# Kernel optimization log

Hardware: AMD Instinct MI355X
Metric: run time of the kernel (lower is better)

The kernel has to match this reference:

```python
import jax, jax.numpy as jnp
import numpy as np

B, H, W, C = 2, 64, 64, 256
NH, K = 8, 7  # num_heads, neighborhood kernel size


def setup_inputs() -> dict:
    key = jax.random.key(0)
    ks = jax.random.split(key, 8)
    xav = lambda k, shape: jax.random.normal(k, shape, jnp.float32) * np.sqrt(2.0 / (shape[0] + shape[1])).astype(np.float32)
    return {
        "x": jax.random.normal(ks[0], (B, H, W, C), jnp.float32),
        "norm1_g": jnp.ones((C,), jnp.float32),
        "norm1_b": jnp.zeros((C,), jnp.float32),
        "qkv_w": xav(ks[1], (3 * C, C)),
        "qkv_b": jnp.zeros((3 * C,), jnp.float32),
        "rpb": jax.random.normal(ks[2], (NH, 2 * K - 1, 2 * K - 1), jnp.float32) * 0.02,
        "proj_w": xav(ks[3], (C, C)),
        "proj_b": jnp.zeros((C,), jnp.float32),
        "norm2_g": jnp.ones((C,), jnp.float32),
        "norm2_b": jnp.zeros((C,), jnp.float32),
        "fc1_w": xav(ks[4], (4 * C, C)),
        "fc1_b": jnp.zeros((4 * C,), jnp.float32),
        "fc2_w": xav(ks[5], (C, 4 * C)),
        "fc2_b": jnp.zeros((C,), jnp.float32),
    }


def _layernorm(x, g, b, eps=1e-5):
    m = x.mean(-1, keepdims=True)
    v = jnp.mean((x - m) ** 2, axis=-1, keepdims=True)
    return (x - m) * jax.lax.rsqrt(v + eps) * g + b


def _nat2d(x, qkv_w, qkv_b, rpb, proj_w, proj_b):
    """Neighborhood attention 2D (NATTEN semantics: edge-clamped k x k windows,
    relative positional bias indexed by key_pos - query_pos + k - 1)."""
    b, h, w, c = x.shape
    nh = rpb.shape[0]
    k = (rpb.shape[1] + 1) // 2
    dh = c // nh
    qkv = (x @ qkv_w.T + qkv_b).reshape(b, h, w, 3, nh, dh)
    q = qkv[..., 0, :, :] * (dh ** -0.5)  # [b,h,w,nh,dh]
    kk = qkv[..., 1, :, :]
    vv = qkv[..., 2, :, :]
    # edge-clamped window starts per query row/col
    starts_h = jnp.clip(jnp.arange(h) - k // 2, 0, h - k)
    starts_w = jnp.clip(jnp.arange(w) - k // 2, 0, w - k)
    idx_h = starts_h[:, None] + jnp.arange(k)  # [h,k] key row indices
    idx_w = starts_w[:, None] + jnp.arange(k)  # [w,k] key col indices
    # gather neighborhoods -> [b,h,w,k,k,nh,dh]
    knb = kk[:, idx_h][:, :, :, idx_w].transpose(0, 1, 3, 2, 4, 5, 6)
    vnb = vv[:, idx_h][:, :, :, idx_w].transpose(0, 1, 3, 2, 4, 5, 6)
    attn = jnp.einsum('bijhd,bijklhd->bijhkl', q, knb)  # [b,h,w,nh,k,k]
    # relative positional bias: index = key - query + (k-1) in [0, 2k-2]
    rb_h = idx_h - jnp.arange(h)[:, None] + (k - 1)  # [h,k]
    rb_w = idx_w - jnp.arange(w)[:, None] + (k - 1)  # [w,k]
    bias = rpb[:, rb_h][:, :, :, rb_w]  # [nh,h,k,w,k]
    bias = bias.transpose(1, 3, 0, 2, 4)  # [h,w,nh,k,k]
    attn = jax.nn.softmax((attn + bias).reshape(b, h, w, nh, k * k), axis=-1)
    out = jnp.einsum('bijhn,bijnhd->bijhd', attn, vnb.reshape(b, h, w, k * k, nh, dh))
    return out.reshape(b, h, w, c) @ proj_w.T + proj_b


def reference(x, norm1_g, norm1_b, qkv_w, qkv_b, rpb, proj_w, proj_b,
              norm2_g, norm2_b, fc1_w, fc1_b, fc2_w, fc2_b):
    # norm -> neighborhood attention -> residual
    x = x + _nat2d(_layernorm(x, norm1_g, norm1_b), qkv_w, qkv_b, rpb, proj_w, proj_b)
    # norm -> MLP (gelu) -> residual
    hdn = _layernorm(x, norm2_g, norm2_b)
    hdn = jax.nn.gelu(hdn @ fc1_w.T + fc1_b, approximate=False)
    return x + (hdn @ fc2_w.T + fc2_b)
```

## Files before the change

### kernel.cpp

```cpp
#include <hip/hip_runtime.h>

typedef __attribute__((ext_vector_type(8))) short bf16x8;
typedef __attribute__((ext_vector_type(4))) float f32x4;
typedef unsigned short u16;

__device__ __forceinline__ float bf2f(u16 u) {
    return __builtin_bit_cast(float, ((unsigned int)u) << 16);
}
__device__ __forceinline__ u16 f2bf(float f) {
    unsigned int x = __builtin_bit_cast(unsigned int, f);
    x += 0x7FFFu + ((x >> 16) & 1u);
    return (u16)(x >> 16);
}

typedef const __attribute__((address_space(1))) void* gas_t;
typedef __attribute__((address_space(3))) void* las_t;
__device__ __forceinline__ void load_lds16(const u16* g, u16* l) {
    __builtin_amdgcn_global_load_lds((gas_t)g, (las_t)l, 16, 0, 0);
}

__global__ __launch_bounds__(256) void prep_kernel(
    const float* __restrict__ s0, const float* __restrict__ s1,
    const float* __restrict__ s2, const float* __restrict__ s3,
    u16* __restrict__ dst,
    const float* __restrict__ x, const float* __restrict__ g,
    const float* __restrict__ b, u16* __restrict__ y)
{
    if (blockIdx.x < 768) {
        const int i4 = (blockIdx.x * 256 + threadIdx.x) * 4;
        const float* src;
        int off;
        if      (i4 < 196608) { src = s0; off = i4; }
        else if (i4 < 262144) { src = s1; off = i4 - 196608; }
        else if (i4 < 524288) { src = s2; off = i4 - 262144; }
        else                  { src = s3; off = i4 - 524288; }
        float4 v = *(const float4*)(src + off);
        ushort4 o;
        o.x = f2bf(v.x); o.y = f2bf(v.y); o.z = f2bf(v.z); o.w = f2bf(v.w);
        *(ushort4*)(dst + i4) = o;
        return;
    }
    const int tok  = (blockIdx.x - 768) * 4 + (threadIdx.x >> 6);
    const int lane = threadIdx.x & 63;
    float4 v = *(const float4*)(x + (size_t)tok * 256 + lane * 4);
    float s  = v.x + v.y + v.z + v.w;
    float sq = v.x*v.x + v.y*v.y + v.z*v.z + v.w*v.w;
    #pragma unroll
    for (int off = 32; off; off >>= 1) {
        s  += __shfl_xor(s, off);
        sq += __shfl_xor(sq, off);
    }
    float mean = s * (1.0f / 256.0f);
    float var  = sq * (1.0f / 256.0f) - mean * mean;
    float rs   = rsqrtf(var + 1e-5f);
    float4 gv = *(const float4*)(g + lane * 4);
    float4 bv = *(const float4*)(b + lane * 4);
    ushort4 o;
    o.x = f2bf((v.x - mean) * rs * gv.x + bv.x);
    o.y = f2bf((v.y - mean) * rs * gv.y + bv.y);
    o.z = f2bf((v.z - mean) * rs * gv.z + bv.z);
    o.w = f2bf((v.w - mean) * rs * gv.w + bv.w);
    *(ushort4*)(y + (size_t)tok * 256 + lane * 4) = o;
}

template<int BM, int BN, int N, int K, int EPI>
__global__ __launch_bounds__(256) void gemm(
    const u16* __restrict__ A, const u16* __restrict__ W,
    const float* __restrict__ bias, const float* __restrict__ res,
    void* __restrict__ outv,
    const float* __restrict__ g2, const float* __restrict__ b2,
    u16* __restrict__ out2)
{
    constexpr int WMT = BM / 32;
    constexpr int WNT = BN / 32;
    constexpr int AR  = BM / 32;
    constexpr int BR  = BN / 32;

    __shared__ u16 As[BM * 64];
    __shared__ u16 Bs[BN * 64];
    __shared__ float red[2][2][16][2];
    const int tid  = threadIdx.x;
    const int lane = tid & 63;
    const int wave = tid >> 6;
    const int m0   = blockIdx.x * BM;
    const int n0   = blockIdx.y * BN;
    const int wm0  = (wave >> 1) * (BM / 2);
    const int wn0  = (wave & 1) * (BN / 2);

    f32x4 acc[WMT][WNT];
    #pragma unroll
    for (int mt = 0; mt < WMT; ++mt)
        #pragma unroll
        for (int nt = 0; nt < WNT; ++nt)
            acc[mt][nt] = (f32x4){0.f, 0.f, 0.f, 0.f};

    int soffA[AR];
    #pragma unroll
    for (int r = 0; r < AR; ++r) {
        const int s   = r * 256 + tid;
        const int row = s >> 3;
        const int c   = (s & 7) ^ (row & 7);
        soffA[r] = row * K + c * 8;
    }
    int soffB[BR];
    #pragma unroll
    for (int r = 0; r < BR; ++r) {
        const int s   = r * 256 + tid;
        const int row = s >> 3;
        const int c   = (s & 7) ^ (row & 7);
        soffB[r] = row * K + c * 8;
    }
    const int fr = lane & 15;
    const int fc = lane >> 4;

    for (int k0 = 0; k0 < K; k0 += 64) {
        __syncthreads();
        #pragma unroll
        for (int r = 0; r < AR; ++r)
            load_lds16(A + (size_t)m0 * K + k0 + soffA[r], As + (r * 256 + tid) * 8);
        #pragma unroll
        for (int r = 0; r < BR; ++r)
            load_lds16(W + (size_t)n0 * K + k0 + soffB[r], Bs + (r * 256 + tid) * 8);
        __syncthreads();
        #pragma unroll
        for (int ks = 0; ks < 2; ++ks) {
            bf16x8 af[WMT], bw[WNT];
            #pragma unroll
            for (int mt = 0; mt < WMT; ++mt) {
                const int rr   = wm0 + mt * 16 + fr;
                const int phys = (ks * 4 + fc) ^ (rr & 7);
                af[mt] = *(const bf16x8*)(As + rr * 64 + phys * 8);
            }
            #pragma unroll
            for (int nt = 0; nt < WNT; ++nt) {
                const int rr   = wn0 + nt * 16 + fr;
                const int phys = (ks * 4 + fc) ^ (rr & 7);
                bw[nt] = *(const bf16x8*)(Bs + rr * 64 + phys * 8);
            }
            #pragma unroll
            for (int mt = 0; mt < WMT; ++mt)
                #pragma unroll
                for (int nt = 0; nt < WNT; ++nt)
                    acc[mt][nt] = __builtin_amdgcn_mfma_f32_16x16x32_bf16(af[mt], bw[nt], acc[mt][nt], 0, 0, 0);
        }
    }

    const int col = lane & 15;
    const int rb  = (lane >> 4) * 4;

    if (EPI == 4) {
        float vv[WNT][4];
        float s[4]  = {0.f, 0.f, 0.f, 0.f};
        float sq[4] = {0.f, 0.f, 0.f, 0.f};
        #pragma unroll
        for (int nt = 0; nt < WNT; ++nt) {
            const int n  = n0 + wn0 + nt * 16 + col;
            const float bv = bias[n];
            #pragma unroll
            for (int r = 0; r < 4; ++r) {
                const int m = m0 + wm0 + rb + r;
                float v = acc[0][nt][r] + bv + res[(size_t)m * N + n];
                ((float*)outv)[(size_t)m * N + n] = v;
                vv[nt][r] = v;
                s[r]  += v;
                sq[r] += v * v;
            }
        }
        #pragma unroll
        for (int off = 1; off < 16; off <<= 1) {
            #pragma unroll
            for (int r = 0; r < 4; ++r) {
                s[r]  += __shfl_xor(s[r], off);
                sq[r] += __shfl_xor(sq[r], off);
            }
        }
        if ((lane & 15) == 0) {
            #pragma unroll
            for (int r = 0; r < 4; ++r) {
                red[wave >> 1][wave & 1][rb + r][0] = s[r];
                red[wave >> 1][wave & 1][rb + r][1] = sq[r];
            }
        }
        __syncthreads();
        float mean[4], rs[4];
        #pragma unroll
        for (int r = 0; r < 4; ++r) {
            float ts  = red[wave >> 1][0][rb + r][0] + red[wave >> 1][1][rb + r][0];
            float tsq = red[wave >> 1][0][rb + r][1] + red[wave >> 1][1][rb + r][1];
            mean[r] = ts * (1.0f / 256.0f);
            float var = tsq * (1.0f / 256.0f) - mean[r] * mean[r];
            rs[r] = rsqrtf(var + 1e-5f);
        }
        #pragma unroll
        for (int nt = 0; nt < WNT; ++nt) {
            const int n  = n0 + wn0 + nt * 16 + col;
            const float gv = g2[n];
            const float bv2 = b2[n];
            #pragma unroll
            for (int r = 0; r < 4; ++r) {
                const int m = m0 + wm0 + rb + r;
                out2[(size_t)m * 256 + n] = f2bf((vv[nt][r] - mean[r]) * rs[r] * gv + bv2);
            }
        }
        return;
    }

    #pragma unroll
    for (int nt = 0; nt < WNT; ++nt) {
        const int n  = n0 + wn0 + nt * 16 + col;
        const float bv = bias[n];
        #pragma unroll
        for (int mt = 0; mt < WMT; ++mt) {
            #pragma unroll
            for (int r = 0; r < 4; ++r) {
                const int m = m0 + wm0 + mt * 16 + rb + r;
                float v = acc[mt][nt][r] + bv;
                if (EPI == 1) {
                    if (n < 256) v *= 0.1767766952966369f;
                    ((u16*)outv)[(size_t)m * N + n] = f2bf(v);
                }
                if (EPI == 2) {
                    v += res[(size_t)m * N + n];
                    ((float*)outv)[(size_t)m * N + n] = v;
                }
                if (EPI == 3) {
                    v = 0.5f * v * (1.0f + erff(v * 0.7071067811865475f));
                    ((u16*)outv)[(size_t)m * N + n] = f2bf(v);
                }
            }
        }
    }
}

__global__ __launch_bounds__(256, 2) void attn_tile_kernel(
    const u16* __restrict__ qkv, const float* __restrict__ rpb,
    u16* __restrict__ out)
{
    __shared__ u16   kv[100 * 64];
    __shared__ u16   qs[16 * 32];
    __shared__ float probs[16 * 66];

    const int tid  = threadIdx.x;
    const int bb   = blockIdx.x >> 8;
    const int rem  = blockIdx.x & 255;
    const int ti0  = (rem >> 4) << 2;
    const int tj0  = (rem & 15) << 2;
    const int oh   = min(max(ti0 - 3, 0), 54);
    const int ow   = min(max(tj0 - 3, 0), 54);
    const int tokbase = bb * 4096;

    int off_kv[4];
    #pragma unroll
    for (int r = 0; r < 4; ++r) {
        const int s  = r * 256 + tid;
        const int t  = s >> 3;
        const int cs = s & 7;
        const int c  = cs ^ (t & 7);
        const int tr = t / 10, tc = t - tr * 10;
        const int tokg = tokbase + (oh + tr) * 64 + (ow + tc);
        off_kv[r] = tokg * 768 + 256 + ((c & 4) << 6) + (c & 3) * 8;
    }
    const int tq   = tid >> 2;
    const int qoff = (tokbase + (ti0 + (tq >> 2)) * 64 + (tj0 + (tq & 3))) * 768
                   + (tid & 3) * 8;

    const int token = tid >> 4;
    const int part  = tid & 15;
    const int li = token >> 2, lj = token & 3;
    const int i  = ti0 + li,   j  = tj0 + lj;
    const int sh = min(max(i - 3, 0), 57);
    const int sw = min(max(j - 3, 0), 57);
    const int rowbase  = (sh - oh) * 10 + (sw - ow);
    const int rb_const = (sh - i + 6) * 13 + (sw - j + 6);
    const size_t outbase = (size_t)(tokbase + i * 64 + j) * 256 + part * 2;

    for (int h = 0; h < 8; ++h) {
        __syncthreads();
        const int hoff = h * 32;
        #pragma unroll
        for (int r = 0; r < 3; ++r)
            load_lds16(qkv + off_kv[r] + hoff, kv + (r * 256 + tid) * 8);
        if (tid < 32)
            load_lds16(qkv + off_kv[3] + hoff, kv + (768 + tid) * 8);
        if (tid < 64)
            load_lds16(qkv + qoff + hoff, qs + tid * 8);
        __syncthreads();

        float qv[32];
        #pragma unroll
        for (int c = 0; c < 4; ++c) {
            bf16x8 v = *(const bf16x8*)(qs + token * 32 + c * 8);
            #pragma unroll
            for (int e = 0; e < 8; ++e) qv[c * 8 + e] = bf2f((u16)v[e]);
        }

        float sc[4];
        #pragma unroll
        for (int sidx = 0; sidx < 4; ++sidx) {
            const int n = part + sidx * 16;
            if (n < 49) {
                const int kh = n / 7, kw = n - (n / 7) * 7;
                const int hidx = rowbase + kh * 10 + kw;
                float acc = rpb[h * 169 + rb_const + kh * 13 + kw];
                #pragma unroll
                for (int c = 0; c < 4; ++c) {
                    const int slot = (hidx << 3) + (c ^ (hidx & 7));
                    bf16x8 kk = *(const bf16x8*)(kv + slot * 8);
                    #pragma unroll
                    for (int e = 0; e < 8; ++e)
                        acc += qv[c * 8 + e] * bf2f((u16)kk[e]);
                }
                sc[sidx] = acc;
            } else {
                sc[sidx] = -1e30f;
            }
        }
        float mx = fmaxf(fmaxf(sc[0], sc[1]), fmaxf(sc[2], sc[3]));
        #pragma unroll
        for (int off = 1; off < 16; off <<= 1) mx = fmaxf(mx, __shfl_xor(mx, off));
        float ex[4], ssum = 0.f;
        #pragma unroll
        for (int sidx = 0; sidx < 4; ++sidx) {
            ex[sidx] = __expf(sc[sidx] - mx);
            ssum += ex[sidx];
        }
        #pragma unroll
        for (int off = 1; off < 16; off <<= 1) ssum += __shfl_xor(ssum, off);
        const float inv = 1.0f / ssum;
        #pragma unroll
        for (int sidx = 0; sidx < 4; ++sidx)
            probs[token * 66 + part + sidx * 16] = ex[sidx] * inv;
        __syncthreads();

        float o0 = 0.f, o1 = 0.f;
        const int vchunk = 4 + (part >> 2);
        const int vsub   = (part & 3) * 2;
        #pragma unroll
        for (int kh = 0; kh < 7; ++kh) {
            #pragma unroll
            for (int kw = 0; kw < 7; ++kw) {
                const int n    = kh * 7 + kw;
                const int hidx = rowbase + kh * 10 + kw;
                const float p  = probs[token * 66 + n];
                const int slot = (hidx << 3) + (vchunk ^ (hidx & 7));
                const unsigned int vv = *(const unsigned int*)(kv + slot * 8 + vsub);
                o0 += p * bf2f((u16)(vv & 0xffffu));
                o1 += p * bf2f((u16)(vv >> 16));
            }
        }
        ushort2 ov;
        ov.x = f2bf(o0); ov.y = f2bf(o1);
        *(ushort2*)(out + outbase + hoff) = ov;
    }
}

extern "C" void kernel_launch(void* const* d_in, const int* in_sizes, int n_in,
                              void* d_out, int out_size, void* d_ws, size_t ws_size,
                              hipStream_t stream)
{
    const float* x      = (const float*)d_in[0];
    const float* n1g    = (const float*)d_in[1];
    const float* n1b    = (const float*)d_in[2];
    const float* qkv_w  = (const float*)d_in[3];
    const float* qkv_b  = (const float*)d_in[4];
    const float* rpb    = (const float*)d_in[5];
    const float* proj_w = (const float*)d_in[6];
    const float* proj_b = (const float*)d_in[7];
    const float* n2g    = (const float*)d_in[8];
    const float* n2b    = (const float*)d_in[9];
    const float* fc1_w  = (const float*)d_in[10];
    const float* fc1_b  = (const float*)d_in[11];
    const float* fc2_w  = (const float*)d_in[12];
    const float* fc2_b  = (const float*)d_in[13];
    float* out = (float*)d_out;

    char* wsb = (char*)d_ws;
    u16*   wbf   = (u16*)wsb;
    u16*   qkvW  = wbf;
    u16*   projW = wbf + 196608;
    u16*   fc1W  = wbf + 262144;
    u16*   fc2W  = wbf + 524288;
    u16*   ln1   = (u16*)(wsb + 1572864);
    u16*   attn  = ln1;
    u16*   qkvB  = (u16*)(wsb + 5767168);
    u16*   ln2   = qkvB;
    u16*   hbuf  = (u16*)(wsb + 9961472);
    float* x1    = (float*)(wsb + 26738688);

    dim3 blk(256);
    prep_kernel<<<2816, blk, 0, stream>>>(qkv_w, proj_w, fc1_w, fc2_w, wbf,
                                          x, n1g, n1b, ln1);
    gemm<64, 64, 768, 256, 1><<<dim3(128, 12), blk, 0, stream>>>(ln1, qkvW, qkv_b, nullptr, qkvB, nullptr, nullptr, nullptr);
    attn_tile_kernel<<<512, blk, 0, stream>>>(qkvB, rpb, attn);
    gemm<32, 256, 256, 256, 4><<<dim3(256, 1), blk, 0, stream>>>(attn, projW, proj_b, x, x1, n2g, n2b, ln2);
    gemm<64, 64, 1024, 256, 3><<<dim3(128, 16), blk, 0, stream>>>(ln2, fc1W, fc1_b, nullptr, hbuf, nullptr, nullptr, nullptr);
    gemm<64, 64, 256, 1024, 2><<<dim3(128, 4), blk, 0, stream>>>(hbuf, fc2W, fc2_b, x1, out, nullptr, nullptr, nullptr);
}
```

Before: 160.1 us.

## Fuse output projection, residual and LayerNorm2 into the attention tile kernel

The attention kernel now keeps its 16-token by 256-channel output in shared memory, using a swizzled layout. It then runs the proj GEMM with MFMA directly from there, reading the proj weights straight from global memory, and applies the bias, residual and LayerNorm2 epilogue before writing x1 and ln2. This removes one kernel launch and the global write and reread of the attention output. In exchange, only 512 blocks each redo a 16x256x256 GEMM with uncached global weight loads, and ln2 moves to a separate workspace region because qkvB can no longer be overwritten.

After: 159.9 us. No clear change (-0.1%).

```diff
diff --git a/kernel.cpp b/kernel.cpp
--- a/kernel.cpp
+++ b/kernel.cpp
@@ -67,9 +67,7 @@
 __global__ __launch_bounds__(256) void gemm(
     const u16* __restrict__ A, const u16* __restrict__ W,
     const float* __restrict__ bias, const float* __restrict__ res,
-    void* __restrict__ outv,
-    const float* __restrict__ g2, const float* __restrict__ b2,
-    u16* __restrict__ out2)
+    void* __restrict__ outv)
 {
     constexpr int WMT = BM / 32;
     constexpr int WNT = BN / 32;
@@ -78,7 +76,6 @@
 
     __shared__ u16 As[BM * 64];
     __shared__ u16 Bs[BN * 64];
-    __shared__ float red[2][2][16][2];
     const int tid  = threadIdx.x;
     const int lane = tid & 63;
     const int wave = tid >> 6;
@@ -147,64 +144,6 @@
 
     const int col = lane & 15;
     const int rb  = (lane >> 4) * 4;
-
-    if (EPI == 4) {
-        float vv[WNT][4];
-        float s[4]  = {0.f, 0.f, 0.f, 0.f};
-        float sq[4] = {0.f, 0.f, 0.f, 0.f};
-        #pragma unroll
-        for (int nt = 0; nt < WNT; ++nt) {
-            const int n  = n0 + wn0 + nt * 16 + col;
-            const float bv = bias[n];
-            #pragma unroll
-            for (int r = 0; r < 4; ++r) {
-                const int m = m0 + wm0 + rb + r;
-                float v = acc[0][nt][r] + bv + res[(size_t)m * N + n];
-                ((float*)outv)[(size_t)m * N + n] = v;
-                vv[nt][r] = v;
-                s[r]  += v;
-                sq[r] += v * v;
-            }
-        }
-        #pragma unroll
-        for (int off = 1; off < 16; off <<= 1) {
-            #pragma unroll
-            for (int r = 0; r < 4; ++r) {
-                s[r]  += __shfl_xor(s[r], off);
-                sq[r] += __shfl_xor(sq[r], off);
-            }
-        }
-        if ((lane & 15) == 0) {
-            #pragma unroll
-            for (int r = 0; r < 4; ++r) {
-                red[wave >> 1][wave & 1][rb + r][0] = s[r];
-                red[wave >> 1][wave & 1][rb + r][1] = sq[r];
-            }
-        }
-        __syncthreads();
-        float mean[4], rs[4];
-        #pragma unroll
-        for (int r = 0; r < 4; ++r) {
-            float ts  = red[wave >> 1][0][rb + r][0] + red[wave >> 1][1][rb + r][0];
-            float tsq = red[wave >> 1][0][rb + r][1] + red[wave >> 1][1][rb + r][1];
-            mean[r] = ts * (1.0f / 256.0f);
-            float var = tsq * (1.0f / 256.0f) - mean[r] * mean[r];
-            rs[r] = rsqrtf(var + 1e-5f);
-        }
-        #pragma unroll
-        for (int nt = 0; nt < WNT; ++nt) {
-            const int n  = n0 + wn0 + nt * 16 + col;
-            const float gv = g2[n];
-            const float bv2 = b2[n];
-            #pragma unroll
-            for (int r = 0; r < 4; ++r) {
-                const int m = m0 + wm0 + rb + r;
-                out2[(size_t)m * 256 + n] = f2bf((vv[nt][r] - mean[r]) * rs[r] * gv + bv2);
-            }
-        }
-        return;
-    }
-
     #pragma unroll
     for (int nt = 0; nt < WNT; ++nt) {
         const int n  = n0 + wn0 + nt * 16 + col;
@@ -232,13 +171,18 @@
     }
 }
 
-__global__ __launch_bounds__(256, 2) void attn_tile_kernel(
+__global__ __launch_bounds__(256, 2) void attn_proj_kernel(
     const u16* __restrict__ qkv, const float* __restrict__ rpb,
-    u16* __restrict__ out)
+    const u16* __restrict__ projW, const float* __restrict__ proj_b,
+    const float* __restrict__ xres, const float* __restrict__ g2,
+    const float* __restrict__ b2, float* __restrict__ x1,
+    u16* __restrict__ ln2)
 {
     __shared__ u16   kv[100 * 64];
     __shared__ u16   qs[16 * 32];
     __shared__ float probs[16 * 66];
+    __shared__ u16   ao[16 * 256];
+    __shared__ float red[4][16][2];
 
     const int tid  = threadIdx.x;
     const int bb   = blockIdx.x >> 8;
@@ -272,7 +216,6 @@
     const int sw = min(max(j - 3, 0), 57);
     const int rowbase  = (sh - oh) * 10 + (sw - ow);
     const int rb_const = (sh - i + 6) * 13 + (sw - j + 6);
-    const size_t outbase = (size_t)(tokbase + i * 64 + j) * 256 + part * 2;
 
     for (int h = 0; h < 8; ++h) {
         __syncthreads();
@@ -350,7 +293,88 @@
         }
         ushort2 ov;
         ov.x = f2bf(o0); ov.y = f2bf(o1);
-        *(ushort2*)(out + outbase + hoff) = ov;
+        const int cch = h * 4 + (part >> 2);
+        const int pch = cch ^ (token & 7);
+        *(ushort2*)(ao + token * 256 + pch * 8 + (part & 3) * 2) = ov;
+    }
+    __syncthreads();
+
+    const int lane = tid & 63;
+    const int wave = tid >> 6;
+    const int fr   = lane & 15;
+    const int fc   = lane >> 4;
+    const int n0w  = wave * 64;
+    f32x4 pacc[4];
+    #pragma unroll
+    for (int nt = 0; nt < 4; ++nt) pacc[nt] = (f32x4){0.f, 0.f, 0.f, 0.f};
+    #pragma unroll
+    for (int ks = 0; ks < 8; ++ks) {
+        const int physA = (ks * 4 + fc) ^ (fr & 7);
+        bf16x8 af = *(const bf16x8*)(ao + fr * 256 + physA * 8);
+        #pragma unroll
+        for (int nt = 0; nt < 4; ++nt) {
+            const int n = n0w + nt * 16 + fr;
+            bf16x8 bw = *(const bf16x8*)(projW + (size_t)n * 256 + ks * 32 + fc * 8);
+            pacc[nt] = __builtin_amdgcn_mfma_f32_16x16x32_bf16(af, bw, pacc[nt], 0, 0, 0);
+        }
+    }
+
+    const int col = lane & 15;
+    const int rb  = (lane >> 4) * 4;
+    float vv[4][4];
+    float s[4]  = {0.f, 0.f, 0.f, 0.f};
+    float sq[4] = {0.f, 0.f, 0.f, 0.f};
+    #pragma unroll
+    for (int nt = 0; nt < 4; ++nt) {
+        const int n = n0w + nt * 16 + col;
+        const float bv = proj_b[n];
+        #pragma unroll
+        for (int r = 0; r < 4; ++r) {
+            const int t = rb + r;
+            const size_t gi = (size_t)(tokbase + (ti0 + (t >> 2)) * 64 + (tj0 + (t & 3))) * 256 + n;
+            float v = pacc[nt][r] + bv + xres[gi];
+            x1[gi] = v;
+            vv[nt][r] = v;
+            s[r]  += v;
+            sq[r] += v * v;
+        }
+    }
+    #pragma unroll
+    for (int off = 1; off < 16; off <<= 1) {
+        #pragma unroll
+        for (int r = 0; r < 4; ++r) {
+            s[r]  += __shfl_xor(s[r], off);
+            sq[r] += __shfl_xor(sq[r], off);
+        }
+    }
+    if (col == 0) {
+        #pragma unroll
+        for (int r = 0; r < 4; ++r) {
+            red[wave][rb + r][0] = s[r];
+            red[wave][rb + r][1] = sq[r];
+        }
+    }
+    __syncthreads();
+    float mean[4], rsv[4];
+    #pragma unroll
+    for (int r = 0; r < 4; ++r) {
+        const float ts = red[0][rb + r][0] + red[1][rb + r][0] + red[2][rb + r][0] + red[3][rb + r][0];
+        const float tq = red[0][rb + r][1] + red[1][rb + r][1] + red[2][rb + r][1] + red[3][rb + r][1];
+        mean[r] = ts * (1.0f / 256.0f);
+        const float var = tq * (1.0f / 256.0f) - mean[r] * mean[r];
+        rsv[r]  = rsqrtf(var + 1e-5f);
+    }
+    #pragma unroll
+    for (int nt = 0; nt < 4; ++nt) {
+        const int n = n0w + nt * 16 + col;
+        const float gv  = g2[n];
+        const float bv2 = b2[n];
+        #pragma unroll
+        for (int r = 0; r < 4; ++r) {
+            const int t = rb + r;
+            const size_t gi = (size_t)(tokbase + (ti0 + (t >> 2)) * 64 + (tj0 + (t & 3))) * 256 + n;
+            ln2[gi] = f2bf((vv[nt][r] - mean[r]) * rsv[r] * gv + bv2);
+        }
     }
 }
 
@@ -381,18 +405,16 @@
     u16*   fc1W  = wbf + 262144;
     u16*   fc2W  = wbf + 524288;
     u16*   ln1   = (u16*)(wsb + 1572864);
-    u16*   attn  = ln1;
     u16*   qkvB  = (u16*)(wsb + 5767168);
-    u16*   ln2   = qkvB;
     u16*   hbuf  = (u16*)(wsb + 9961472);
     float* x1    = (float*)(wsb + 26738688);
+    u16*   ln2   = (u16*)(wsb + 35651584);
 
     dim3 blk(256);
     prep_kernel<<<2816, blk, 0, stream>>>(qkv_w, proj_w, fc1_w, fc2_w, wbf,
                                           x, n1g, n1b, ln1);
-    gemm<64, 64, 768, 256, 1><<<dim3(128, 12), blk, 0, stream>>>(ln1, qkvW, qkv_b, nullptr, qkvB, nullptr, nullptr, nullptr);
-    attn_tile_kernel<<<512, blk, 0, stream>>>(qkvB, rpb, attn);
-    gemm<32, 256, 256, 256, 4><<<dim3(256, 1), blk, 0, stream>>>(attn, projW, proj_b, x, x1, n2g, n2b, ln2);
-    gemm<64, 64, 1024, 256, 3><<<dim3(128, 16), blk, 0, stream>>>(ln2, fc1W, fc1_b, nullptr, hbuf, nullptr, nullptr, nullptr);
-    gemm<64, 64, 256, 1024, 2><<<dim3(128, 4), blk, 0, stream>>>(hbuf, fc2W, fc2_b, x1, out, nullptr, nullptr, nullptr);
-}
+    gemm<64, 64, 768, 256, 1><<<dim3(128, 12), blk, 0, stream>>>(ln1, qkvW, qkv_b, nullptr, qkvB);
+    attn_proj_kernel<<<512, blk, 0, stream>>>(qkvB, rpb, projW, proj_b, x, n2g, n2b, x1, ln2);
+    gemm<64, 64, 1024, 256, 3><<<dim3(128, 16), blk, 0, stream>>>(ln2, fc1W, fc1_b, nullptr, hbuf);
+    gemm<64, 64, 256, 1024, 2><<<dim3(128, 4), blk, 0, stream>>>(hbuf, fc2W, fc2_b, x1, out);
+}
```

## Rewrite neighborhood attention as per-head single-wave MFMA kernel over 10x10 key tiles

Applied to the files above, without the earlier changes.

Replaces the scalar-FMA attention kernel, which looped over 8 heads per 256-thread block, with a 64-thread kernel that handles one (4x4 query tile, head) pair. QK scores over the full 10x10 key patch are computed with bf16 MFMA, and out-of-window keys are masked through the bias lookup. PV is also done with MFMA, using a hi/lo bf16 split of the probabilities to keep precision. K and V are read straight from global memory with no LDS staging, and a grid remap interleaves heads across blocks. The trade is wasted MFMA work on masked keys plus scattered 2-byte V gathers, in exchange for removing the scalar dot-product loops and the per-head block synchronisation.

New measurement: 151.3 us. 5.5% less time.

```diff
diff --git a/kernel.cpp b/kernel.cpp
--- a/kernel.cpp
+++ b/kernel.cpp
@@ -232,125 +232,134 @@
     }
 }
 
-__global__ __launch_bounds__(256, 2) void attn_tile_kernel(
+__global__ __launch_bounds__(64) void attn_mfma_kernel(
     const u16* __restrict__ qkv, const float* __restrict__ rpb,
     u16* __restrict__ out)
 {
-    __shared__ u16   kv[100 * 64];
-    __shared__ u16   qs[16 * 32];
-    __shared__ float probs[16 * 66];
-
-    const int tid  = threadIdx.x;
-    const int bb   = blockIdx.x >> 8;
-    const int rem  = blockIdx.x & 255;
+    __shared__ float rpbs[192];
+
+    const int l = threadIdx.x;
+    const int B = blockIdx.x;
+    const int L = (B & 7) * 512 + (B >> 3);
+    const int tile = L >> 3;
+    const int h    = L & 7;
+    const int bb   = tile >> 8;
+    const int rem  = tile & 255;
     const int ti0  = (rem >> 4) << 2;
     const int tj0  = (rem & 15) << 2;
     const int oh   = min(max(ti0 - 3, 0), 54);
     const int ow   = min(max(tj0 - 3, 0), 54);
     const int tokbase = bb * 4096;
 
-    int off_kv[4];
+    #pragma unroll
+    for (int r = 0; r < 3; ++r) {
+        const int idx = r * 64 + l;
+        rpbs[idx] = (idx < 169) ? rpb[h * 169 + idx] : -1e30f;
+    }
+
+    const int q = l & 15;
+    const int g = l >> 4;
+
+    const int tokq = tokbase + (ti0 + (q >> 2)) * 64 + (tj0 + (q & 3));
+    const bf16x8 qf = *(const bf16x8*)(qkv + (size_t)tokq * 768 + h * 32 + g * 8);
+    bf16x8 kf[7];
+    #pragma unroll
+    for (int t = 0; t < 7; ++t) {
+        const int key = 16 * t + q;
+        const int kkc = min(key, 99);
+        const int tr  = (kkc * 205) >> 11, tc = kkc - tr * 10;
+        const int tokg = tokbase + (oh + tr) * 64 + (ow + tc);
+        kf[t] = *(const bf16x8*)(qkv + (size_t)tokg * 768 + 256 + h * 32 + g * 8);
+    }
+
+    const int i  = ti0 + (q >> 2), j = tj0 + (q & 3);
+    const int sh = min(max(i - 3, 0), 57), sw = min(max(j - 3, 0), 57);
+    const int khb = sh - oh, kwb = sw - ow;
+    const int bh0 = oh - i + 6, bw0 = ow - j + 6;
+    int bidx[7][4];
+    int vtok[7][4];
+    #pragma unroll
+    for (int t = 0; t < 7; ++t)
+        #pragma unroll
+        for (int r = 0; r < 4; ++r) {
+            const int kk  = 16 * t + 4 * g + r;
+            const int kkc = min(kk, 99);
+            const int hr  = (kkc * 205) >> 11;
+            const int hc  = kkc - hr * 10;
+            vtok[t][r] = tokbase + (oh + hr) * 64 + (ow + hc);
+            const bool valid = (kk < 100)
+                && ((unsigned)(hr - khb) < 7u) && ((unsigned)(hc - kwb) < 7u);
+            bidx[t][r] = valid ? (bh0 + hr) * 13 + (bw0 + hc) : 169;
+        }
+
+    __syncthreads();
+
+    f32x4 S[7];
+    #pragma unroll
+    for (int t = 0; t < 7; ++t)
+        S[t] = __builtin_amdgcn_mfma_f32_16x16x32_bf16(kf[t], qf, (f32x4){0.f,0.f,0.f,0.f}, 0, 0, 0);
+
+    float p[7][4];
+    float mx = -1e30f;
+    #pragma unroll
+    for (int t = 0; t < 7; ++t)
+        #pragma unroll
+        for (int r = 0; r < 4; ++r) {
+            const float v = S[t][r] + rpbs[bidx[t][r]];
+            p[t][r] = v;
+            mx = fmaxf(mx, v);
+        }
+    mx = fmaxf(mx, __shfl_xor(mx, 16));
+    mx = fmaxf(mx, __shfl_xor(mx, 32));
+    float sum = 0.f;
+    #pragma unroll
+    for (int t = 0; t < 7; ++t)
+        #pragma unroll
+        for (int r = 0; r < 4; ++r) {
+            const float e = __expf(p[t][r] - mx);
+            p[t][r] = e;
+            sum += e;
+        }
+    sum += __shfl_xor(sum, 16);
+    sum += __shfl_xor(sum, 32);
+    const float inv = 1.f / sum;
+
+    f32x4 O0 = {0.f,0.f,0.f,0.f}, O1 = {0.f,0.f,0.f,0.f};
+    const u16* vbase = qkv + 512 + h * 32 + q;
+    #pragma unroll
+    for (int kt = 0; kt < 4; ++kt) {
+        const int t0   = 2 * kt;
+        const bool has1 = (2 * kt + 1) < 7;
+        const int t1   = has1 ? 2 * kt + 1 : 2 * kt;
+        bf16x8 ph, pl, vA, vB;
+        #pragma unroll
+        for (int jj = 0; jj < 4; ++jj) {
+            const float a = p[t0][jj] * inv;
+            const u16 ha = f2bf(a);
+            ph[jj] = (short)ha;
+            pl[jj] = (short)f2bf(a - bf2f(ha));
+            const float b = has1 ? p[t1][jj] * inv : 0.f;
+            const u16 hb = f2bf(b);
+            ph[4 + jj] = (short)hb;
+            pl[4 + jj] = (short)f2bf(b - bf2f(hb));
+            vA[jj]     = (short)vbase[(size_t)vtok[t0][jj] * 768];
+            vB[jj]     = (short)vbase[(size_t)vtok[t0][jj] * 768 + 16];
+            vA[4 + jj] = (short)vbase[(size_t)vtok[t1][jj] * 768];
+            vB[4 + jj] = (short)vbase[(size_t)vtok[t1][jj] * 768 + 16];
+        }
+        O0 = __builtin_amdgcn_mfma_f32_16x16x32_bf16(ph, vA, O0, 0, 0, 0);
+        O0 = __builtin_amdgcn_mfma_f32_16x16x32_bf16(pl, vA, O0, 0, 0, 0);
+        O1 = __builtin_amdgcn_mfma_f32_16x16x32_bf16(ph, vB, O1, 0, 0, 0);
+        O1 = __builtin_amdgcn_mfma_f32_16x16x32_bf16(pl, vB, O1, 0, 0, 0);
+    }
+
     #pragma unroll
     for (int r = 0; r < 4; ++r) {
-        const int s  = r * 256 + tid;
-        const int t  = s >> 3;
-        const int cs = s & 7;
-        const int c  = cs ^ (t & 7);
-        const int tr = t / 10, tc = t - tr * 10;
-        const int tokg = tokbase + (oh + tr) * 64 + (ow + tc);
-        off_kv[r] = tokg * 768 + 256 + ((c & 4) << 6) + (c & 3) * 8;
-    }
-    const int tq   = tid >> 2;
-    const int qoff = (tokbase + (ti0 + (tq >> 2)) * 64 + (tj0 + (tq & 3))) * 768
-                   + (tid & 3) * 8;
-
-    const int token = tid >> 4;
-    const int part  = tid & 15;
-    const int li = token >> 2, lj = token & 3;
-    const int i  = ti0 + li,   j  = tj0 + lj;
-    const int sh = min(max(i - 3, 0), 57);
-    const int sw = min(max(j - 3, 0), 57);
-    const int rowbase  = (sh - oh) * 10 + (sw - ow);
-    const int rb_const = (sh - i + 6) * 13 + (sw - j + 6);
-    const size_t outbase = (size_t)(tokbase + i * 64 + j) * 256 + part * 2;
-
-    for (int h = 0; h < 8; ++h) {
-        __syncthreads();
-        const int hoff = h * 32;
-        #pragma unroll
-        for (int r = 0; r < 3; ++r)
-            load_lds16(qkv + off_kv[r] + hoff, kv + (r * 256 + tid) * 8);
-        if (tid < 32)
-            load_lds16(qkv + off_kv[3] + hoff, kv + (768 + tid) * 8);
-        if (tid < 64)
-            load_lds16(qkv + qoff + hoff, qs + tid * 8);
-        __syncthreads();
-
-        float qv[32];
-        #pragma unroll
-        for (int c = 0; c < 4; ++c) {
-            bf16x8 v = *(const bf16x8*)(qs + token * 32 + c * 8);
-            #pragma unroll
-            for (int e = 0; e < 8; ++e) qv[c * 8 + e] = bf2f((u16)v[e]);
-        }
-
-        float sc[4];
-        #pragma unroll
-        for (int sidx = 0; sidx < 4; ++sidx) {
-            const int n = part + sidx * 16;
-            if (n < 49) {
-                const int kh = n / 7, kw = n - (n / 7) * 7;
-                const int hidx = rowbase + kh * 10 + kw;
-                float acc = rpb[h * 169 + rb_const + kh * 13 + kw];
-                #pragma unroll
-                for (int c = 0; c < 4; ++c) {
-                    const int slot = (hidx << 3) + (c ^ (hidx & 7));
-                    bf16x8 kk = *(const bf16x8*)(kv + slot * 8);
-                    #pragma unroll
-                    for (int e = 0; e < 8; ++e)
-                        acc += qv[c * 8 + e] * bf2f((u16)kk[e]);
-                }
-                sc[sidx] = acc;
-            } else {
-                sc[sidx] = -1e30f;
-            }
-        }
-        float mx = fmaxf(fmaxf(sc[0], sc[1]), fmaxf(sc[2], sc[3]));
-        #pragma unroll
-        for (int off = 1; off < 16; off <<= 1) mx = fmaxf(mx, __shfl_xor(mx, off));
-        float ex[4], ssum = 0.f;
-        #pragma unroll
-        for (int sidx = 0; sidx < 4; ++sidx) {
-            ex[sidx] = __expf(sc[sidx] - mx);
-            ssum += ex[sidx];
-        }
-        #pragma unroll
-        for (int off = 1; off < 16; off <<= 1) ssum += __shfl_xor(ssum, off);
-        const float inv = 1.0f / ssum;
-        #pragma unroll
-        for (int sidx = 0; sidx < 4; ++sidx)
-            probs[token * 66 + part + sidx * 16] = ex[sidx] * inv;
-        __syncthreads();
-
-        float o0 = 0.f, o1 = 0.f;
-        const int vchunk = 4 + (part >> 2);
-        const int vsub   = (part & 3) * 2;
-        #pragma unroll
-        for (int kh = 0; kh < 7; ++kh) {
-            #pragma unroll
-            for (int kw = 0; kw < 7; ++kw) {
-                const int n    = kh * 7 + kw;
-                const int hidx = rowbase + kh * 10 + kw;
-                const float p  = probs[token * 66 + n];
-                const int slot = (hidx << 3) + (vchunk ^ (hidx & 7));
-                const unsigned int vv = *(const unsigned int*)(kv + slot * 8 + vsub);
-                o0 += p * bf2f((u16)(vv & 0xffffu));
-                o1 += p * bf2f((u16)(vv >> 16));
-            }
-        }
-        ushort2 ov;
-        ov.x = f2bf(o0); ov.y = f2bf(o1);
-        *(ushort2*)(out + outbase + hoff) = ov;
+        const int qq = g * 4 + r;
+        const size_t base = (size_t)(tokbase + (ti0 + (qq >> 2)) * 64 + (tj0 + (qq & 3))) * 256
+                          + h * 32 + q;
+        out[base]      = f2bf(O0[r]);
+        out[base + 16] = f2bf(O1[r]);
     }
 }
 
@@ -391,7 +400,7 @@
     prep_kernel<<<2816, blk, 0, stream>>>(qkv_w, proj_w, fc1_w, fc2_w, wbf,
                                           x, n1g, n1b, ln1);
     gemm<64, 64, 768, 256, 1><<<dim3(128, 12), blk, 0, stream>>>(ln1, qkvW, qkv_b, nullptr, qkvB, nullptr, nullptr, nullptr);
-    attn_tile_kernel<<<512, blk, 0, stream>>>(qkvB, rpb, attn);
+    attn_mfma_kernel<<<4096, dim3(64), 0, stream>>>(qkvB, rpb, attn);
     gemm<32, 256, 256, 256, 4><<<dim3(256, 1), blk, 0, stream>>>(attn, projW, proj_b, x, x1, n2g, n2b, ln2);
     gemm<64, 64, 1024, 256, 3><<<dim3(128, 16), blk, 0, stream>>>(ln2, fc1W, fc1_b, nullptr, hbuf, nullptr, nullptr, nullptr);
     gemm<64, 64, 256, 1024, 2><<<dim3(128, 4), blk, 0, stream>>>(hbuf, fc2W, fc2_b, x1, out, nullptr, nullptr, nullptr);
```
